# Optimization experiments

Measured on AMD Instinct MI355X. Metric: run time of the kernel, lower is better.

## Reference

```python
import jax, jax.numpy as jnp
import numpy as np

B, T, C = 2, 2048, 2048
NH, NKV = 16, 4
HD = C // NH  # 128


def _rope(x, cos, sin):
    d = x.shape[-1] // 2
    x1, x2 = x[..., :d], x[..., d:]
    return jnp.concatenate([x1 * cos + x2 * sin, -x1 * sin + x2 * cos], axis=-1)


def _rmsnorm(x):
    eps = jnp.finfo(x.dtype).eps
    return x * jax.lax.rsqrt(jnp.mean(jnp.square(x), axis=-1, keepdims=True) + eps)


def setup_inputs() -> dict:
    key = jax.random.key(0)
    ks = jax.random.split(key, 7)
    s = 0.02
    return {
        "x": jax.random.normal(ks[0], (B, T, C), jnp.float32),
        "cos": jax.random.normal(ks[1], (1, T, 1, HD // 2), jnp.float32),
        "sin": jax.random.normal(ks[2], (1, T, 1, HD // 2), jnp.float32),
        "wq": jax.random.normal(ks[3], (C, NH * HD), jnp.float32) * s,
        "wk": jax.random.normal(ks[4], (C, NKV * HD), jnp.float32) * s,
        "wv": jax.random.normal(ks[5], (C, NKV * HD), jnp.float32) * s,
        "wo": jax.random.normal(ks[6], (C, C), jnp.float32) * s,
    }


def reference(x, cos, sin, wq, wk, wv, wo):
    q = (x @ wq).reshape(B, T, NH, HD)
    k = (x @ wk).reshape(B, T, NKV, HD)
    v = (x @ wv).reshape(B, T, NKV, HD)
    q = _rmsnorm(_rope(q, cos, sin))
    k = _rmsnorm(_rope(k, cos, sin))
    # [B, H, T, D]
    q = q.transpose(0, 2, 1, 3)
    k = k.transpose(0, 2, 1, 3)
    v = v.transpose(0, 2, 1, 3)
    rep = NH // NKV
    k = jnp.repeat(k, rep, axis=1)
    v = jnp.repeat(v, rep, axis=1)
    scale = 1.0 / jnp.sqrt(jnp.float32(HD))
    scores = jnp.einsum("bhqd,bhkd->bhqk", q, k) * scale
    causal = jnp.tril(jnp.ones((T, T), bool))
    scores = jnp.where(causal, scores, jnp.finfo(scores.dtype).min)
    attn = jax.nn.softmax(scores, axis=-1)
    y = jnp.einsum("bhqk,bhkd->bhqd", attn, v)
    y = y.transpose(0, 2, 1, 3).reshape(B, T, C)
    return y @ wo
```

## Files before the change

### kernel.cpp

```cpp
#include <hip/hip_runtime.h>
#include <hip/hip_bf16.h>
#include <cstdint>

typedef unsigned short u16;
typedef __bf16 bf16x8 __attribute__((ext_vector_type(8)));
typedef float f32x4 __attribute__((ext_vector_type(4)));
typedef unsigned short u16x8 __attribute__((ext_vector_type(8)));
typedef unsigned short u16x4 __attribute__((ext_vector_type(4)));

#define B_ 2
#define T_ 2048
#define C_ 2048
#define NH_ 16
#define NKV_ 4
#define HD_ 128
#define K2_ 0.12752004650581538f

__device__ __forceinline__ u16 f2bf(float f) {
    unsigned u = __builtin_bit_cast(unsigned, f);
    unsigned r = u + 0x7FFFu + ((u >> 16) & 1u);
    return (u16)(r >> 16);
}

__device__ __forceinline__ void gl16(const void* g, void* l) {
    auto gp = reinterpret_cast<const __attribute__((address_space(1))) unsigned*>(
        reinterpret_cast<uintptr_t>(g));
    auto lp = reinterpret_cast<__attribute__((address_space(3))) unsigned*>(
        reinterpret_cast<uintptr_t>(l));
    __builtin_amdgcn_global_load_lds(gp, lp, 16, 0, 0);
}

__global__ void transpose_conv(const float* __restrict__ in, u16* __restrict__ out, int N) {
    __shared__ float tile[32][33];
    int n0 = blockIdx.x * 32, k0 = blockIdx.y * 32;
    int tx = threadIdx.x, ty = threadIdx.y;
#pragma unroll
    for (int i = 0; i < 4; ++i)
        tile[ty * 4 + i][tx] = in[(size_t)(k0 + ty * 4 + i) * N + n0 + tx];
    __syncthreads();
#pragma unroll
    for (int i = 0; i < 4; ++i)
        out[(size_t)(n0 + ty * 4 + i) * 2048 + k0 + tx] = f2bf(tile[tx][ty * 4 + i]);
}

__global__ void convert4(const float4* __restrict__ in, u16* __restrict__ out) {
    int i = blockIdx.x * 256 + threadIdx.x;
    float4 v = in[i];
    u16x4 o;
    o[0] = f2bf(v.x); o[1] = f2bf(v.y); o[2] = f2bf(v.z); o[3] = f2bf(v.w);
    ((u16x4*)out)[i] = o;
}

__global__ __launch_bounds__(256, 2) void gemm_bf16(const u16* __restrict__ A,
                                                    const u16* __restrict__ BT,
                                                    float* __restrict__ C, int N, int K) {
    __shared__ __align__(16) u16 As[128 * 64];
    __shared__ __align__(16) u16 Bs[128 * 64];
    int t = threadIdx.x;
    int w = t >> 6, l = t & 63;
    int wr = w >> 1, wc = w & 1;
    int lg = l >> 4, lr = l & 15;
    int m0 = blockIdx.y * 128, n0 = blockIdx.x * 128;
    f32x4 acc[4][4] = {};

    int ar = t >> 3;
    int acb = (t & 7) * 16;
    const char* Abase = (const char*)(A + (size_t)(m0 + ar) * K) + acb;
    const char* Bbase = (const char*)(BT + (size_t)(n0 + ar) * K) + acb;
    char* AsB = (char*)As + t * 16;
    char* BsB = (char*)Bs + t * 16;

    for (int kt = 0; kt < K; kt += 64) {
        if (kt) __syncthreads();
#pragma unroll
        for (int i = 0; i < 4; ++i) {
            gl16(Abase + (size_t)(i * 32) * K * 2 + (size_t)kt * 2, AsB + i * 4096);
            gl16(Bbase + (size_t)(i * 32) * K * 2 + (size_t)kt * 2, BsB + i * 4096);
        }
        __syncthreads();
#pragma unroll
        for (int kk = 0; kk < 2; ++kk) {
            bf16x8 af[4], bfr[4];
#pragma unroll
            for (int m = 0; m < 4; ++m)
                af[m] = *(const bf16x8*)(As + (wr * 64 + m * 16 + lr) * 64 + kk * 32 + lg * 8);
#pragma unroll
            for (int n = 0; n < 4; ++n)
                bfr[n] = *(const bf16x8*)(Bs + (wc * 64 + n * 16 + lr) * 64 + kk * 32 + lg * 8);
#pragma unroll
            for (int m = 0; m < 4; ++m)
#pragma unroll
                for (int n = 0; n < 4; ++n)
                    acc[m][n] = __builtin_amdgcn_mfma_f32_16x16x32_bf16(af[m], bfr[n], acc[m][n], 0, 0, 0);
        }
    }
#pragma unroll
    for (int m = 0; m < 4; ++m) {
        int row = m0 + wr * 64 + m * 16 + lg * 4;
#pragma unroll
        for (int n = 0; n < 4; ++n) {
            int col = n0 + wc * 64 + n * 16 + lr;
            float* Cp = C + (size_t)row * N + col;
#pragma unroll
            for (int r = 0; r < 4; ++r)
                Cp[(size_t)r * N] = acc[m][n][r];
        }
    }
}

__global__ void rope_rms(const float* __restrict__ qkv, const float* __restrict__ cs,
                         const float* __restrict__ sn, u16* __restrict__ qh,
                         u16* __restrict__ kh) {
    int task = blockIdx.x * 4 + (threadIdx.x >> 6);
    int l = threadIdx.x & 63;
    const float* in;
    u16* out;
    int tpos;
    float post = 1.0f;
    if (task < 65536) {
        int row = task >> 4, h = task & 15;
        in = qkv + (size_t)row * 3072 + h * 128;
        int b = row >> 11; tpos = row & 2047;
        out = qh + ((size_t)(b * NH_ + h) * T_ + tpos) * HD_;
        post = K2_;
    } else {
        int t2 = task - 65536;
        int row = t2 >> 2, h = t2 & 3;
        in = qkv + (size_t)row * 3072 + 2048 + h * 128;
        int b = row >> 11; tpos = row & 2047;
        out = kh + ((size_t)(b * NKV_ + h) * T_ + tpos) * HD_;
    }
    float x1 = in[l], x2 = in[l + 64];
    float c = cs[tpos * 64 + l], s = sn[tpos * 64 + l];
    float o1 = x1 * c + x2 * s;
    float o2 = -x1 * s + x2 * c;
    float ss = o1 * o1 + o2 * o2;
#pragma unroll
    for (int m = 1; m < 64; m <<= 1) ss += __shfl_xor(ss, m);
    float r = rsqrtf(ss * (1.0f / 128.0f) + 1.1920929e-07f) * post;
    out[l] = f2bf(o1 * r);
    out[l + 64] = f2bf(o2 * r);
}

__global__ void transpose_v(const float* __restrict__ qkv, u16* __restrict__ vt) {
    __shared__ float tile[32][33];
    int t0 = blockIdx.x * 32;
    int d0 = blockIdx.y * 32;
    int bk = blockIdx.z;
    int b = bk >> 2, kvh = bk & 3;
    int tx = threadIdx.x, ty = threadIdx.y;
#pragma unroll
    for (int i = 0; i < 4; ++i)
        tile[ty * 4 + i][tx] =
            qkv[(size_t)(b * 2048 + t0 + ty * 4 + i) * 3072 + 2560 + kvh * 128 + d0 + tx];
    __syncthreads();
#pragma unroll
    for (int i = 0; i < 4; ++i)
        vt[((size_t)bk * 128 + d0 + ty * 4 + i) * 2048 + t0 + tx] = f2bf(tile[tx][ty * 4 + i]);
}

__global__ __launch_bounds__(512, 1) void attn(const u16* __restrict__ Q,
                                               const u16* __restrict__ Kk,
                                               const u16* __restrict__ V,
                                               u16* __restrict__ Y) {
    extern __shared__ __align__(16) u16 sm[];
    u16* Ks = sm;
    u16* Vs = sm + 16384;
    u16* Pb = sm + 32768;

    int bid = blockIdx.x;
    int xcd = bid & 7;
    int b = xcd >> 2, kvh = xcd & 3;
    int sp2 = bid >> 3;
    int t = threadIdx.x;
    int w = t >> 6, l = t & 63;
    int lg = l >> 4, lr = l & 15;
    int h = kvh * 4 + (w & 3);
    int j = sp2 * 2 + (w >> 2);
    int qwA = j * 16, qwB = (127 - j) * 16;
    int NA = j / 4 + 1;

    const u16* Qp = Q + (size_t)(b * NH_ + h) * T_ * HD_;
    const u16* Kp = Kk + (size_t)(b * NKV_ + kvh) * T_ * HD_;
    const u16* Vp = V + (size_t)(b * NKV_ + kvh) * HD_ * T_;
    u16* Yp = Y + (size_t)(b * T_) * 2048 + h * HD_;
    u16* Pw = Pb + w * 1152;

    int g0 = t, g1 = t + 512;
    auto stage = [&](int kv0, int buf) {
        const char* Kb = (const char*)Kp + (size_t)kv0 * 256;
        const char* Vb = (const char*)Vp + (size_t)kv0 * 2;
        char* Kd = (char*)(Ks + buf * 8192);
        char* Vd = (char*)(Vs + buf * 8192);
        gl16(Kb + (g0 >> 4) * 256 + (((g0 & 15) ^ ((g0 >> 4) & 15)) * 16), Kd + g0 * 16);
        gl16(Kb + (g1 >> 4) * 256 + (((g1 & 15) ^ ((g1 >> 4) & 15)) * 16), Kd + g1 * 16);
        gl16(Vb + (size_t)(g0 >> 3) * 4096 + (((g0 & 7) ^ ((g0 >> 3) & 7)) * 16), Vd + g0 * 16);
        gl16(Vb + (size_t)(g1 >> 3) * 4096 + (((g1 & 7) ^ ((g1 >> 3) & 7)) * 16), Vd + g1 * 16);
    };

    bf16x8 aq[4];
    auto loadQ = [&](int qw2) {
#pragma unroll
        for (int ch = 0; ch < 4; ++ch)
            aq[ch] = *(const bf16x8*)(Qp + (size_t)(qw2 + lr) * HD_ + ch * 32 + lg * 8);
    };

    f32x4 acc[8] = {};
    float m2[4], lp_[4];
#pragma unroll
    for (int r = 0; r < 4; ++r) { m2[r] = -1e30f; lp_[r] = 0.0f; }

    auto epi = [&](int qw2) {
#pragma unroll
        for (int r = 0; r < 4; ++r) {
            float lt = lp_[r];
            lt += __shfl_xor(lt, 1);
            lt += __shfl_xor(lt, 2);
            lt += __shfl_xor(lt, 4);
            lt += __shfl_xor(lt, 8);
            float inv = 1.0f / lt;
#pragma unroll
            for (int oc = 0; oc < 8; ++oc)
                Yp[(size_t)(qw2 + lg * 4 + r) * 2048 + oc * 16 + lr] = f2bf(acc[oc][r] * inv);
        }
    };

    loadQ(qwA);
    int qw = qwA;
    stage(0, 0);

    for (int gi = 0; gi < 33; ++gi) {
        asm volatile("s_waitcnt vmcnt(0)" ::: "memory");
        __builtin_amdgcn_s_barrier();
        __builtin_amdgcn_sched_barrier(0);
        int cur = gi & 1;
        if (gi < 32) {
            int gn = gi + 1;
            stage((gn < NA ? gn : gn - NA) * 64, cur ^ 1);
        }
        if (gi == NA) {
            epi(qwA);
#pragma unroll
            for (int oc = 0; oc < 8; ++oc) acc[oc] = f32x4{0.f, 0.f, 0.f, 0.f};
#pragma unroll
            for (int r = 0; r < 4; ++r) { m2[r] = -1e30f; lp_[r] = 0.0f; }
            loadQ(qwB);
            qw = qwB;
        }
        int kv0 = (gi < NA ? gi : gi - NA) * 64;
        int kbase = cur * 8192;

        f32x4 sc[4] = {};
        __builtin_amdgcn_s_setprio(1);
#pragma unroll
        for (int ch = 0; ch < 4; ++ch)
#pragma unroll
            for (int kf = 0; kf < 4; ++kf) {
                bf16x8 bk = *(const bf16x8*)&Ks[kbase + (kf * 16 + lr) * 128 + (((ch * 4 + lg) ^ lr) * 8)];
                sc[kf] = __builtin_amdgcn_mfma_f32_16x16x32_bf16(aq[ch], bk, sc[kf], 0, 0, 0);
            }
        __builtin_amdgcn_s_setprio(0);

        bf16x8 bv[16];
#pragma unroll
        for (int oc = 0; oc < 8; ++oc)
#pragma unroll
            for (int kk = 0; kk < 2; ++kk)
                bv[oc * 2 + kk] = *(const bf16x8*)&Vs[kbase + (oc * 16 + lr) * 64 +
                                                     (((kk * 4 + lg) ^ (lr & 7)) * 8)];

        bool nm = (kv0 + 63 >= qw);
        float sv[4][4], mx[4];
#pragma unroll
        for (int r = 0; r < 4; ++r) {
            int row = qw + lg * 4 + r;
#pragma unroll
            for (int kf = 0; kf < 4; ++kf) {
                float x = sc[kf][r];
                if (nm) {
                    int key = kv0 + kf * 16 + lr;
                    x = (key > row) ? -1e38f : x;
                }
                sv[r][kf] = x;
            }
            mx[r] = fmaxf(fmaxf(sv[r][0], sv[r][1]), fmaxf(sv[r][2], sv[r][3]));
        }
#pragma unroll
        for (int r = 0; r < 4; ++r) {
            float m = mx[r];
            m = fmaxf(m, __shfl_xor(m, 1));
            m = fmaxf(m, __shfl_xor(m, 2));
            m = fmaxf(m, __shfl_xor(m, 4));
            m = fmaxf(m, __shfl_xor(m, 8));
            mx[r] = m;
        }
        bool upd = false;
#pragma unroll
        for (int r = 0; r < 4; ++r) upd |= (mx[r] > m2[r] + 8.0f);
        if (__any(upd)) {
#pragma unroll
            for (int r = 0; r < 4; ++r) {
                float mn = fmaxf(m2[r], mx[r]);
                float rs = exp2f(m2[r] - mn);
                m2[r] = mn;
                lp_[r] *= rs;
#pragma unroll
                for (int oc = 0; oc < 8; ++oc) acc[oc] *= rs;
            }
        }
#pragma unroll
        for (int r = 0; r < 4; ++r) {
            float m = m2[r];
            float ps = 0.0f;
#pragma unroll
            for (int kf = 0; kf < 4; ++kf) {
                float p = exp2f(sv[r][kf] - m);
                ps += p;
                Pw[(lg * 4 + r) * 72 + kf * 16 + lr] = f2bf(p);
            }
            lp_[r] += ps;
        }
        bf16x8 ap[2];
#pragma unroll
        for (int kk = 0; kk < 2; ++kk)
            ap[kk] = *(const bf16x8*)&Pw[lr * 72 + kk * 32 + lg * 8];
        __builtin_amdgcn_s_setprio(1);
#pragma unroll
        for (int oc = 0; oc < 8; ++oc)
#pragma unroll
            for (int kk = 0; kk < 2; ++kk)
                acc[oc] = __builtin_amdgcn_mfma_f32_16x16x32_bf16(ap[kk], bv[oc * 2 + kk], acc[oc], 0, 0, 0);
        __builtin_amdgcn_s_setprio(0);
    }
    epi(qwB);
}

extern "C" void kernel_launch(void* const* d_in, const int* in_sizes, int n_in,
                              void* d_out, int out_size, void* d_ws, size_t ws_size,
                              hipStream_t stream) {
    const float* x    = (const float*)d_in[0];
    const float* cosT = (const float*)d_in[1];
    const float* sinT = (const float*)d_in[2];
    const float* wq   = (const float*)d_in[3];
    const float* wk   = (const float*)d_in[4];
    const float* wv   = (const float*)d_in[5];
    const float* wo   = (const float*)d_in[6];
    float* out = (float*)d_out;

    char* ws = (char*)d_ws;
    u16*   wqkvT = (u16*)(ws);
    u16*   woT   = (u16*)(ws + 12582912);
    u16*   xb    = (u16*)(ws + 20971520);
    float* qkv   = (float*)(ws + 37748736);
    u16*   qh    = (u16*)(ws + 88080384);
    u16*   kh    = (u16*)(ws + 104857600);
    u16*   vt    = (u16*)(ws + 109051904);
    u16*   y     = xb;

    static int smem_set = 0;
    if (!smem_set) {
        hipFuncSetAttribute(reinterpret_cast<const void*>(&attn),
                            hipFuncAttributeMaxDynamicSharedMemorySize, 83968);
        smem_set = 1;
    }

    transpose_conv<<<dim3(64, 64), dim3(32, 8), 0, stream>>>(wq, wqkvT, 2048);
    transpose_conv<<<dim3(16, 64), dim3(32, 8), 0, stream>>>(wk, wqkvT + (size_t)2048 * 2048, 512);
    transpose_conv<<<dim3(16, 64), dim3(32, 8), 0, stream>>>(wv, wqkvT + (size_t)2560 * 2048, 512);
    transpose_conv<<<dim3(64, 64), dim3(32, 8), 0, stream>>>(wo, woT, 2048);
    convert4<<<8192, 256, 0, stream>>>((const float4*)x, xb);

    gemm_bf16<<<dim3(24, 32), 256, 0, stream>>>(xb, wqkvT, qkv, 3072, 2048);

    rope_rms<<<20480, 256, 0, stream>>>(qkv, cosT, sinT, qh, kh);
    transpose_v<<<dim3(64, 4, 8), dim3(32, 8), 0, stream>>>(qkv, vt);

    attn<<<256, 512, 83968, stream>>>(qh, kh, vt, y);

    gemm_bf16<<<dim3(16, 32), 256, 0, stream>>>(y, woT, out, 2048, 2048);
}
```

Measured before the change: 236.7 us.

## Restructure attention to 256-thread blocks with transposed S layout and packed P writes

The attention kernel moves from 512-thread blocks (one per CU) to 256-thread blocks with two per CU. The QK^T MFMA operands are swapped so each lane holds one query row, which reduces softmax state to a scalar per lane and cuts the shuffle reductions. P is converted with packed bf16 conversion and written as 8-byte stores, and V fragments are loaded just before use instead of being preloaded into 16 registers. The GEMM also gets an XCD-aware block remapping to improve L2 locality. The costs are a larger grid, fewer waves sharing each staged K/V tile, and a hipFuncSetAttribute call on every launch.

After: 225.6 us. 1.05x faster.

```diff
diff --git a/kernel.cpp b/kernel.cpp
--- a/kernel.cpp
+++ b/kernel.cpp
@@ -5,8 +5,8 @@
 typedef unsigned short u16;
 typedef __bf16 bf16x8 __attribute__((ext_vector_type(8)));
 typedef float f32x4 __attribute__((ext_vector_type(4)));
-typedef unsigned short u16x8 __attribute__((ext_vector_type(8)));
 typedef unsigned short u16x4 __attribute__((ext_vector_type(4)));
+typedef unsigned uint2v __attribute__((ext_vector_type(2)));
 
 #define B_ 2
 #define T_ 2048
@@ -22,6 +22,12 @@
     return (u16)(r >> 16);
 }
 
+__device__ __forceinline__ unsigned cvtpk(float a, float b) {
+    unsigned r;
+    asm("v_cvt_pk_bf16_f32 %0, %1, %2" : "=v"(r) : "v"(a), "v"(b));
+    return r;
+}
+
 __device__ __forceinline__ void gl16(const void* g, void* l) {
     auto gp = reinterpret_cast<const __attribute__((address_space(1))) unsigned*>(
         reinterpret_cast<uintptr_t>(g));
@@ -56,20 +62,23 @@
                                                     float* __restrict__ C, int N, int K) {
     __shared__ __align__(16) u16 As[128 * 64];
     __shared__ __align__(16) u16 Bs[128 * 64];
+    int nwg = gridDim.x * gridDim.y;
+    int bid = blockIdx.y * gridDim.x + blockIdx.x;
+    int nb = (bid & 7) * (nwg >> 3) + (bid >> 3);
+    int bx = nb % gridDim.x, by = nb / gridDim.x;
+
     int t = threadIdx.x;
     int w = t >> 6, l = t & 63;
     int wr = w >> 1, wc = w & 1;
     int lg = l >> 4, lr = l & 15;
-    int m0 = blockIdx.y * 128, n0 = blockIdx.x * 128;
+    int m0 = by * 128, n0 = bx * 128;
     f32x4 acc[4][4] = {};
-
     int ar = t >> 3;
     int acb = (t & 7) * 16;
     const char* Abase = (const char*)(A + (size_t)(m0 + ar) * K) + acb;
     const char* Bbase = (const char*)(BT + (size_t)(n0 + ar) * K) + acb;
     char* AsB = (char*)As + t * 16;
     char* BsB = (char*)Bs + t * 16;
-
     for (int kt = 0; kt < K; kt += 64) {
         if (kt) __syncthreads();
 #pragma unroll
@@ -159,7 +168,7 @@
         vt[((size_t)bk * 128 + d0 + ty * 4 + i) * 2048 + t0 + tx] = f2bf(tile[tx][ty * 4 + i]);
 }
 
-__global__ __launch_bounds__(512, 1) void attn(const u16* __restrict__ Q,
+__global__ __launch_bounds__(256, 2) void attn(const u16* __restrict__ Q,
                                                const u16* __restrict__ Kk,
                                                const u16* __restrict__ V,
                                                u16* __restrict__ Y) {
@@ -171,12 +180,11 @@
     int bid = blockIdx.x;
     int xcd = bid & 7;
     int b = xcd >> 2, kvh = xcd & 3;
-    int sp2 = bid >> 3;
+    int j = bid >> 3;
     int t = threadIdx.x;
     int w = t >> 6, l = t & 63;
     int lg = l >> 4, lr = l & 15;
-    int h = kvh * 4 + (w & 3);
-    int j = sp2 * 2 + (w >> 2);
+    int h = kvh * 4 + w;
     int qwA = j * 16, qwB = (127 - j) * 16;
     int NA = j / 4 + 1;
 
@@ -186,16 +194,17 @@
     u16* Yp = Y + (size_t)(b * T_) * 2048 + h * HD_;
     u16* Pw = Pb + w * 1152;
 
-    int g0 = t, g1 = t + 512;
     auto stage = [&](int kv0, int buf) {
         const char* Kb = (const char*)Kp + (size_t)kv0 * 256;
         const char* Vb = (const char*)Vp + (size_t)kv0 * 2;
         char* Kd = (char*)(Ks + buf * 8192);
         char* Vd = (char*)(Vs + buf * 8192);
-        gl16(Kb + (g0 >> 4) * 256 + (((g0 & 15) ^ ((g0 >> 4) & 15)) * 16), Kd + g0 * 16);
-        gl16(Kb + (g1 >> 4) * 256 + (((g1 & 15) ^ ((g1 >> 4) & 15)) * 16), Kd + g1 * 16);
-        gl16(Vb + (size_t)(g0 >> 3) * 4096 + (((g0 & 7) ^ ((g0 >> 3) & 7)) * 16), Vd + g0 * 16);
-        gl16(Vb + (size_t)(g1 >> 3) * 4096 + (((g1 & 7) ^ ((g1 >> 3) & 7)) * 16), Vd + g1 * 16);
+#pragma unroll
+        for (int i = 0; i < 4; ++i) {
+            int g = t + i * 256;
+            gl16(Kb + (g >> 4) * 256 + (((g & 15) ^ ((g >> 4) & 15)) * 16), Kd + g * 16);
+            gl16(Vb + (size_t)(g >> 3) * 4096 + (((g & 7) ^ ((g >> 3) & 7)) * 16), Vd + g * 16);
+        }
     };
 
     bf16x8 aq[4];
@@ -206,23 +215,21 @@
     };
 
     f32x4 acc[8] = {};
-    float m2[4], lp_[4];
-#pragma unroll
-    for (int r = 0; r < 4; ++r) { m2[r] = -1e30f; lp_[r] = 0.0f; }
+    float m2 = -1e30f, lpS = 0.0f;
 
     auto epi = [&](int qw2) {
-#pragma unroll
-        for (int r = 0; r < 4; ++r) {
-            float lt = lp_[r];
-            lt += __shfl_xor(lt, 1);
-            lt += __shfl_xor(lt, 2);
-            lt += __shfl_xor(lt, 4);
-            lt += __shfl_xor(lt, 8);
-            float inv = 1.0f / lt;
-#pragma unroll
-            for (int oc = 0; oc < 8; ++oc)
-                Yp[(size_t)(qw2 + lg * 4 + r) * 2048 + oc * 16 + lr] = f2bf(acc[oc][r] * inv);
-        }
+        float lt = lpS;
+        lt += __shfl_xor(lt, 16);
+        lt += __shfl_xor(lt, 32);
+        float inv = 1.0f / lt;
+        float inv4[4];
+#pragma unroll
+        for (int r = 0; r < 4; ++r) inv4[r] = __shfl(inv, 4 * lg + r, 16);
+#pragma unroll
+        for (int oc = 0; oc < 8; ++oc)
+#pragma unroll
+            for (int r = 0; r < 4; ++r)
+                Yp[(size_t)(qw2 + 4 * lg + r) * 2048 + oc * 16 + lr] = f2bf(acc[oc][r] * inv4[r]);
     };
 
     loadQ(qwA);
@@ -242,8 +249,7 @@
             epi(qwA);
 #pragma unroll
             for (int oc = 0; oc < 8; ++oc) acc[oc] = f32x4{0.f, 0.f, 0.f, 0.f};
-#pragma unroll
-            for (int r = 0; r < 4; ++r) { m2[r] = -1e30f; lp_[r] = 0.0f; }
+            m2 = -1e30f; lpS = 0.0f;
             loadQ(qwB);
             qw = qwB;
         }
@@ -257,79 +263,71 @@
 #pragma unroll
             for (int kf = 0; kf < 4; ++kf) {
                 bf16x8 bk = *(const bf16x8*)&Ks[kbase + (kf * 16 + lr) * 128 + (((ch * 4 + lg) ^ lr) * 8)];
-                sc[kf] = __builtin_amdgcn_mfma_f32_16x16x32_bf16(aq[ch], bk, sc[kf], 0, 0, 0);
+                sc[kf] = __builtin_amdgcn_mfma_f32_16x16x32_bf16(bk, aq[ch], sc[kf], 0, 0, 0);
             }
         __builtin_amdgcn_s_setprio(0);
 
-        bf16x8 bv[16];
+        int qrow = qw + lr;
+        bool nm = (kv0 + 63 > qw);
+        if (nm) {
+#pragma unroll
+            for (int kf = 0; kf < 4; ++kf)
+#pragma unroll
+                for (int r = 0; r < 4; ++r) {
+                    int key = kv0 + kf * 16 + 4 * lg + r;
+                    if (key > qrow) sc[kf][r] = -1e38f;
+                }
+        }
+        float mk[4];
+#pragma unroll
+        for (int kf = 0; kf < 4; ++kf)
+            mk[kf] = fmaxf(fmaxf(sc[kf][0], sc[kf][1]), fmaxf(sc[kf][2], sc[kf][3]));
+        float mx = fmaxf(fmaxf(mk[0], mk[1]), fmaxf(mk[2], mk[3]));
+        mx = fmaxf(mx, __shfl_xor(mx, 16));
+        mx = fmaxf(mx, __shfl_xor(mx, 32));
+
+        if (__any(mx > m2 + 8.0f)) {
+            float mn = fmaxf(m2, mx);
+            float rs = exp2f(m2 - mn);
+            m2 = mn;
+            lpS *= rs;
+            float rs4[4];
+#pragma unroll
+            for (int r = 0; r < 4; ++r) rs4[r] = __shfl(rs, 4 * lg + r, 16);
+#pragma unroll
+            for (int oc = 0; oc < 8; ++oc)
+#pragma unroll
+                for (int r = 0; r < 4; ++r) acc[oc][r] *= rs4[r];
+        }
+
+        float ps = 0.0f;
+#pragma unroll
+        for (int kf = 0; kf < 4; ++kf) {
+            float p0 = exp2f(sc[kf][0] - m2);
+            float p1 = exp2f(sc[kf][1] - m2);
+            float p2 = exp2f(sc[kf][2] - m2);
+            float p3 = exp2f(sc[kf][3] - m2);
+            ps += (p0 + p1) + (p2 + p3);
+            uint2v pk;
+            pk[0] = cvtpk(p0, p1);
+            pk[1] = cvtpk(p2, p3);
+            *(uint2v*)&Pw[lr * 72 + kf * 16 + 4 * lg] = pk;
+        }
+        lpS += ps;
+
+        bf16x8 ap[2];
+#pragma unroll
+        for (int kk = 0; kk < 2; ++kk)
+            ap[kk] = *(const bf16x8*)&Pw[lr * 72 + kk * 32 + 8 * lg];
+        __builtin_amdgcn_s_setprio(1);
 #pragma unroll
         for (int oc = 0; oc < 8; ++oc)
 #pragma unroll
-            for (int kk = 0; kk < 2; ++kk)
-                bv[oc * 2 + kk] = *(const bf16x8*)&Vs[kbase + (oc * 16 + lr) * 64 +
-                                                     (((kk * 4 + lg) ^ (lr & 7)) * 8)];
-
-        bool nm = (kv0 + 63 >= qw);
-        float sv[4][4], mx[4];
-#pragma unroll
-        for (int r = 0; r < 4; ++r) {
-            int row = qw + lg * 4 + r;
-#pragma unroll
-            for (int kf = 0; kf < 4; ++kf) {
-                float x = sc[kf][r];
-                if (nm) {
-                    int key = kv0 + kf * 16 + lr;
-                    x = (key > row) ? -1e38f : x;
-                }
-                sv[r][kf] = x;
+            for (int kk = 0; kk < 2; ++kk) {
+                bf16x8 bv = *(const bf16x8*)&Vs[kbase + (oc * 16 + lr) * 64 +
+                                                (((kk * 4 + lg) ^ (lr & 7)) * 8)];
+                acc[oc] = __builtin_amdgcn_mfma_f32_16x16x32_bf16(ap[kk], bv, acc[oc], 0, 0, 0);
             }
-            mx[r] = fmaxf(fmaxf(sv[r][0], sv[r][1]), fmaxf(sv[r][2], sv[r][3]));
-        }
-#pragma unroll
-        for (int r = 0; r < 4; ++r) {
-            float m = mx[r];
-            m = fmaxf(m, __shfl_xor(m, 1));
-            m = fmaxf(m, __shfl_xor(m, 2));
-            m = fmaxf(m, __shfl_xor(m, 4));
-            m = fmaxf(m, __shfl_xor(m, 8));
-            mx[r] = m;
-        }
-        bool upd = false;
-#pragma unroll
-        for (int r = 0; r < 4; ++r) upd |= (mx[r] > m2[r] + 8.0f);
-        if (__any(upd)) {
-#pragma unroll
-            for (int r = 0; r < 4; ++r) {
-                float mn = fmaxf(m2[r], mx[r]);
-                float rs = exp2f(m2[r] - mn);
-                m2[r] = mn;
-                lp_[r] *= rs;
-#pragma unroll
-                for (int oc = 0; oc < 8; ++oc) acc[oc] *= rs;
-            }
-        }
-#pragma unroll
-        for (int r = 0; r < 4; ++r) {
-            float m = m2[r];
-            float ps = 0.0f;
-#pragma unroll
-            for (int kf = 0; kf < 4; ++kf) {
-                float p = exp2f(sv[r][kf] - m);
-                ps += p;
-                Pw[(lg * 4 + r) * 72 + kf * 16 + lr] = f2bf(p);
-            }
-            lp_[r] += ps;
-        }
-        bf16x8 ap[2];
-#pragma unroll
-        for (int kk = 0; kk < 2; ++kk)
-            ap[kk] = *(const bf16x8*)&Pw[lr * 72 + kk * 32 + lg * 8];
-        __builtin_amdgcn_s_setprio(1);
-#pragma unroll
-        for (int oc = 0; oc < 8; ++oc)
-#pragma unroll
-            for (int kk = 0; kk < 2; ++kk)
-                acc[oc] = __builtin_amdgcn_mfma_f32_16x16x32_bf16(ap[kk], bv[oc * 2 + kk], acc[oc], 0, 0, 0);
         __builtin_amdgcn_s_setprio(0);
     }
     epi(qwB);
@@ -357,12 +355,8 @@
     u16*   vt    = (u16*)(ws + 109051904);
     u16*   y     = xb;
 
-    static int smem_set = 0;
-    if (!smem_set) {
-        hipFuncSetAttribute(reinterpret_cast<const void*>(&attn),
-                            hipFuncAttributeMaxDynamicSharedMemorySize, 83968);
-        smem_set = 1;
-    }
+    hipFuncSetAttribute(reinterpret_cast<const void*>(&attn),
+                        hipFuncAttributeMaxDynamicSharedMemorySize, 74752);
 
     transpose_conv<<<dim3(64, 64), dim3(32, 8), 0, stream>>>(wq, wqkvT, 2048);
     transpose_conv<<<dim3(16, 64), dim3(32, 8), 0, stream>>>(wk, wqkvT + (size_t)2048 * 2048, 512);
@@ -375,7 +369,7 @@
     rope_rms<<<20480, 256, 0, stream>>>(qkv, cosT, sinT, qh, kh);
     transpose_v<<<dim3(64, 4, 8), dim3(32, 8), 0, stream>>>(qkv, vt);
 
-    attn<<<256, 512, 83968, stream>>>(qh, kh, vt, y);
+    attn<<<512, 256, 74752, stream>>>(qh, kh, vt, y);
 
     gemm_bf16<<<dim3(16, 32), 256, 0, stream>>>(y, woT, out, 2048, 2048);
 }
```
